# Performance work log

Hardware: AMD Instinct MI355X
Metric: run time of the kernel (lower is better)

The kernel has to match this reference:

```python
import jax, jax.numpy as jnp
import numpy as np


def _banded_diag_mean(a, b, r):
    """For each (batch i, row j) return mean of (a[i] @ b[i].T)[j, j-r:j+r+1],
    computed without materializing the LxL matrix. Windows are clipped to
    [max(0,j-r), min(L, j+r+1)].  a, b: [B, L, D]."""
    B, L, _ = a.shape
    sums = jnp.zeros((B, L), a.dtype)
    counts = jnp.zeros((L,), a.dtype)
    for d in range(-r, r + 1):  # small fixed set of 2r+1 diagonals
        if d >= 0:
            dots = jnp.einsum('bld,bld->bl', a[:, :L - d], b[:, d:])
            sums = sums.at[:, :L - d].add(dots)
            counts = counts.at[:L - d].add(1.0)
        else:
            dots = jnp.einsum('bld,bld->bl', a[:, -d:], b[:, :L + d])
            sums = sums.at[:, -d:].add(dots)
            counts = counts.at[-d:].add(1.0)
    return sums / counts


def setup_inputs() -> dict:
    key = jax.random.key(0)
    k1, k2, k3 = jax.random.split(key, 3)
    B, L, D_in, D_feat = 8, 1024, 512, 256
    return {
        'feature1': jax.random.normal(k1, (B, L, D_in), jnp.float32),
        'feature2': jax.random.normal(k2, (B, L, D_in), jnp.float32),
        'W': jax.random.normal(k3, (D_in, D_feat), jnp.float32) / np.sqrt(D_in),
        'b': jnp.zeros((D_feat,), jnp.float32),
        'positive_range_self': 4,
        'positive_range_tgt': 4,
    }


def reference(feature1, feature2, W, b, positive_range_self, positive_range_tgt):
    # MLPLayer projection (shared eval_func for both inputs): linear + relu
    emb_1 = jax.nn.relu(feature1 @ W + b)  # [B, L, Df]
    emb_2 = jax.nn.relu(feature2 @ W + b)  # [B, L, Df]
    B, L, Df = emb_1.shape
    N = B * L

    positive = jnp.einsum('bld,bld->bl', emb_1, emb_2)  # [B, L]
    if positive_range_self > 0:
        positive = positive + _banded_diag_mean(emb_1, emb_1, positive_range_self)
        positive = positive + _banded_diag_mean(emb_2, emb_2, positive_range_self)
    if positive_range_tgt > 0:
        positive = positive + _banded_diag_mean(emb_1, emb_2, positive_range_tgt)
    positive = positive.reshape(N)

    e1 = emb_1.reshape(N, Df)
    e2 = emb_2.reshape(N, Df)
    sim_matrix = e1 @ e2.T  # [N, N]
    negative = jax.nn.logsumexp(sim_matrix, axis=-1) - jnp.log(jnp.asarray(N, sim_matrix.dtype))

    nce_loss = jnp.mean(-positive + negative)
    return nce_loss
```

## Files before the change

### kernel.cpp

```cpp
#include <hip/hip_runtime.h>
#include <hip/hip_bf16.h>
#include <math.h>

#define DIN 512
#define DF 256
#define LSEQ 1024
#define NTOT 8192

typedef __attribute__((ext_vector_type(8))) short short8;
typedef __attribute__((ext_vector_type(4))) short short4v;
typedef __attribute__((ext_vector_type(4))) float f32x4;

__device__ __forceinline__ short f2bf(float x) {
  union { float f; unsigned u; } un; un.f = x;
  unsigned r = un.u + 0x7fffu + ((un.u >> 16) & 1u);
  return (short)(r >> 16);
}
__device__ __forceinline__ float bf2f(short s) {
  union { unsigned u; float f; } un; un.u = ((unsigned)(unsigned short)s) << 16;
  return un.f;
}

typedef __attribute__((address_space(1))) const unsigned char AS1c;
typedef __attribute__((address_space(3))) unsigned char AS3;
__device__ __forceinline__ void gload16(const void* g, void* l) {
  __builtin_amdgcn_global_load_lds((AS1c*)g, (AS3*)l, 16, 0, 0);
}
#define CFENCE() asm volatile("" ::: "memory")
#define LN2 0.69314718056f

__global__ __launch_bounds__(256) void prep_w_kernel(const float* __restrict__ W,
                                                     short* __restrict__ Wt) {
  __shared__ short t[64 * 70];
  const int tid = threadIdx.x;
  const int k0 = (blockIdx.x & 7) * 64;
  const int c0 = (blockIdx.x >> 3) * 64;
  const int cl = tid & 63, kq = tid >> 6;
#pragma unroll
  for (int r = 0; r < 16; ++r) {
    int kl = kq * 16 + r;
    t[cl * 70 + kl] = f2bf(W[(size_t)(k0 + kl) * DF + c0 + cl]);
  }
  __syncthreads();
  const int kl2 = tid & 63, cq = tid >> 6;
#pragma unroll
  for (int r = 0; r < 16; ++r) {
    int cl2 = cq * 16 + r;
    Wt[(size_t)(c0 + cl2) * DIN + k0 + kl2] = t[cl2 * 70 + kl2];
  }
}

#define PBM 64
#define PBK 64

__global__ __launch_bounds__(256) void proj_kernel(const float* __restrict__ f1,
                                                   const float* __restrict__ f2,
                                                   const short* __restrict__ Wt,
                                                   const float* __restrict__ bias,
                                                   short* __restrict__ emb1,
                                                   short* __restrict__ emb2) {
  const float* feat = blockIdx.y ? f2 : f1;
  short* emb = blockIdx.y ? emb2 : emb1;
  __shared__ short ldsA[8 * 64 * 8];
  __shared__ short ldsB[8 * 256 * 8];
  const int tid = threadIdx.x;
  const int lane = tid & 63, wv = tid >> 6;
  const int wrow = (wv & 1) * 32, wcol = (wv >> 1) * 128;
  const int l15 = lane & 15, lk16 = lane >> 4;
  const int rowbase = blockIdx.x * PBM;

  f32x4 acc[2][8];
#pragma unroll
  for (int mi = 0; mi < 2; ++mi)
#pragma unroll
    for (int nf = 0; nf < 8; ++nf) acc[mi][nf] = f32x4{0.f, 0.f, 0.f, 0.f};

  for (int K0 = 0; K0 < DIN; K0 += PBK) {
    __syncthreads();
#pragma unroll
    for (int i = 0; i < 8; ++i)
      gload16(Wt + (size_t)tid * DIN + K0 + i * 8, ldsB + (i * 256 + tid) * 8);
#pragma unroll
    for (int i = 0; i < 2; ++i) {
      int g = i * 256 + tid;
      int kb = g >> 6, r = g & 63;
      const float* src = feat + (size_t)(rowbase + r) * DIN + K0 + kb * 8;
      f32x4 v0 = *(const f32x4*)(src);
      f32x4 v1 = *(const f32x4*)(src + 4);
      short8 h;
      h[0] = f2bf(v0[0]); h[1] = f2bf(v0[1]); h[2] = f2bf(v0[2]); h[3] = f2bf(v0[3]);
      h[4] = f2bf(v1[0]); h[5] = f2bf(v1[1]); h[6] = f2bf(v1[2]); h[7] = f2bf(v1[3]);
      *(short8*)(ldsA + g * 8) = h;
    }
    __syncthreads();
#pragma unroll
    for (int kk = 0; kk < 2; ++kk) {
      const int kb = kk * 4 + lk16;
      short8 af[2], bf[8];
#pragma unroll
      for (int mi = 0; mi < 2; ++mi)
        af[mi] = *(const short8*)(ldsA + (kb * 64 + wrow + mi * 16 + l15) * 8);
#pragma unroll
      for (int nf = 0; nf < 8; ++nf)
        bf[nf] = *(const short8*)(ldsB + (kb * 256 + wcol + nf * 16 + l15) * 8);
#pragma unroll
      for (int mi = 0; mi < 2; ++mi)
#pragma unroll
        for (int nf = 0; nf < 8; ++nf)
          acc[mi][nf] = __builtin_amdgcn_mfma_f32_16x16x32_bf16(af[mi], bf[nf], acc[mi][nf], 0, 0, 0);
    }
  }
  const int r4 = (lane >> 4) * 4;
#pragma unroll
  for (int mi = 0; mi < 2; ++mi) {
    int row0 = rowbase + wrow + mi * 16 + r4;
#pragma unroll
    for (int nf = 0; nf < 8; ++nf) {
      int col = wcol + nf * 16 + l15;
      float bb = bias[col];
#pragma unroll
      for (int r = 0; r < 4; ++r) {
        float v = acc[mi][nf][r] + bb;
        v = v > 0.f ? v : 0.f;
        emb[(size_t)(row0 + r) * DF + col] = f2bf(v);
      }
    }
  }
}

#define POSR 32
#define PSTR 258

__global__ __launch_bounds__(256) void positive_kernel(const short* __restrict__ emb1,
                                                       const short* __restrict__ emb2,
                                                       const int* __restrict__ prs,
                                                       const int* __restrict__ prt,
                                                       float* __restrict__ pos) {
  __shared__ short s1[40 * PSTR];
  __shared__ short s2[40 * PSTR];
  const int tid = threadIdx.x;
  const int b = blockIdx.x >> 5;
  const int j0 = (blockIdx.x & 31) * POSR;
  const int rs = prs[0], rt = prt[0];

  {
    const int rr = tid >> 6, c4 = (tid & 63) * 4;
#pragma unroll
    for (int it = 0; it < 10; ++it) {
      int r = it * 4 + rr;
      int g = j0 - 4 + r;
      short4v v1 = short4v{0, 0, 0, 0}, v2 = short4v{0, 0, 0, 0};
      if (g >= 0 && g < LSEQ) {
        size_t off = (size_t)(b * LSEQ + g) * DF + c4;
        v1 = *(const short4v*)(emb1 + off);
        v2 = *(const short4v*)(emb2 + off);
      }
      *(short4v*)(s1 + r * PSTR + c4) = v1;
      *(short4v*)(s2 + r * PSTR + c4) = v2;
    }
  }
  __syncthreads();

  const int lane = tid & 63, wv = tid >> 6;
  for (int q = 0; q < 8; ++q) {
    const int j = j0 + wv * 8 + q;
    const int rl = wv * 8 + q + 4;
    float a1[4], a2[4];
    {
      short4v v1 = *(const short4v*)(s1 + rl * PSTR + lane * 4);
      short4v v2 = *(const short4v*)(s2 + rl * PSTR + lane * 4);
#pragma unroll
      for (int i = 0; i < 4; ++i) { a1[i] = bf2f(v1[i]); a2[i] = bf2f(v2[i]); }
    }
    float dot12 = 0.f, p11 = 0.f, p22 = 0.f, p12 = 0.f;
#pragma unroll
    for (int i = 0; i < 4; ++i) dot12 += a1[i] * a2[i];
    int rmax = rs > rt ? rs : rt;
    for (int d = -rmax; d <= rmax; ++d) {
      int k = j + d;
      if (k < 0 || k >= LSEQ) continue;
      int kl = rl + d;
      short4v w1 = *(const short4v*)(s1 + kl * PSTR + lane * 4);
      short4v w2 = *(const short4v*)(s2 + kl * PSTR + lane * 4);
      float d11 = 0.f, d22 = 0.f, d12 = 0.f;
#pragma unroll
      for (int i = 0; i < 4; ++i) {
        float e1k = bf2f(w1[i]), e2k = bf2f(w2[i]);
        d11 += a1[i] * e1k;
        d22 += a2[i] * e2k;
        d12 += a1[i] * e2k;
      }
      if (d >= -rs && d <= rs) { p11 += d11; p22 += d22; }
      if (d >= -rt && d <= rt) { p12 += d12; }
    }
#pragma unroll
    for (int m = 1; m < 64; m <<= 1) {
      dot12 += __shfl_xor(dot12, m);
      p11 += __shfl_xor(p11, m);
      p22 += __shfl_xor(p22, m);
      p12 += __shfl_xor(p12, m);
    }
    if (lane == 0) {
      float res = dot12;
      if (rs > 0) {
        int lo = j - rs < 0 ? 0 : j - rs;
        int hi = j + rs > LSEQ - 1 ? LSEQ - 1 : j + rs;
        res += (p11 + p22) / (float)(hi - lo + 1);
      }
      if (rt > 0) {
        int lo = j - rt < 0 ? 0 : j - rt;
        int hi = j + rt > LSEQ - 1 ? LSEQ - 1 : j + rt;
        res += p12 / (float)(hi - lo + 1);
      }
      pos[b * LSEQ + j] = res;
    }
  }
}

#define NBM 128
#define NBN 32
#define NCHUNK 16
#define CHW (NTOT / NCHUNK)
#define NT (CHW / NBN)

__global__ __launch_bounds__(256, 3) void negative_kernel(const short* __restrict__ e1,
                                                          const short* __restrict__ e2,
                                                          float* __restrict__ mpart,
                                                          float* __restrict__ spart) {
  __shared__ short ldsB[2][NBN * DF];
  const int tid = threadIdx.x;
  const int lane = tid & 63, wv = tid >> 6;
  const int l15 = lane & 15, lk16 = lane >> 4;
  const int rowbase = blockIdx.x * NBM + wv * 32;
  const short* colbase = e2 + (size_t)(blockIdx.y * CHW) * DF;

  const int src_off = (tid & 31) * DF + (tid >> 5) * 8;
  const int dst_off = wv * 512;

  auto stage = [&](int tt) {
    const short* nb = colbase + (size_t)tt * NBN * DF + src_off;
    short* db = (short*)ldsB[tt & 1] + dst_off;
#pragma unroll
    for (int i = 0; i < 4; ++i)
      gload16(nb + i * 64, db + i * 2048);
  };

  stage(0);
  CFENCE();
  short8 a[2][8];
#pragma unroll
  for (int mi = 0; mi < 2; ++mi)
#pragma unroll
    for (int ks = 0; ks < 8; ++ks)
      a[mi][ks] = *(const short8*)(e1 + (size_t)(rowbase + mi * 16 + l15) * DF + ks * 32 + lk16 * 8);
  CFENCE();
  stage(1);
  CFENCE();

  float mrun[8], srun[8];
#pragma unroll
  for (int i = 0; i < 8; ++i) { mrun[i] = -1e30f; srun[i] = 0.f; }

  for (int t = 0; t < NT; ++t) {
    if (t < NT - 1) asm volatile("s_waitcnt vmcnt(4)" ::: "memory");
    else            asm volatile("s_waitcnt vmcnt(0)" ::: "memory");
    __builtin_amdgcn_s_barrier();
    const short* bbase = (const short*)ldsB[t & 1] + lk16 * 256 + l15 * 8;

    f32x4 acc[2][2];
#pragma unroll
    for (int mi = 0; mi < 2; ++mi)
#pragma unroll
      for (int nf = 0; nf < 2; ++nf) acc[mi][nf] = f32x4{0.f, 0.f, 0.f, 0.f};

    __builtin_amdgcn_s_setprio(1);
#pragma unroll
    for (int ks = 0; ks < 8; ++ks) {
      short8 b0 = *(const short8*)(bbase + ks * 1024);
      short8 b1 = *(const short8*)(bbase + ks * 1024 + 128);
#pragma unroll
      for (int mi = 0; mi < 2; ++mi) {
        acc[mi][0] = __builtin_amdgcn_mfma_f32_16x16x32_bf16(a[mi][ks], b0, acc[mi][0], 0, 0, 0);
        acc[mi][1] = __builtin_amdgcn_mfma_f32_16x16x32_bf16(a[mi][ks], b1, acc[mi][1], 0, 0, 0);
      }
    }
    __builtin_amdgcn_s_setprio(0);

#pragma unroll
    for (int mi = 0; mi < 2; ++mi)
#pragma unroll
      for (int r = 0; r < 4; ++r) {
        int s8 = mi * 4 + r;
        float v0 = acc[mi][0][r], v1 = acc[mi][1][r];
        float mo = mrun[s8];
        float mn = fmaxf(mo, fmaxf(v0, v1));
        mrun[s8] = mn;
        srun[s8] = srun[s8] * __expf(mo - mn) + __expf(v0 - mn) + __expf(v1 - mn);
      }
    __builtin_amdgcn_s_barrier();
    CFENCE();
    if (t + 2 < NT) stage(t + 2);
  }

#pragma unroll
  for (int mi = 0; mi < 2; ++mi)
#pragma unroll
    for (int r = 0; r < 4; ++r) {
      int s8 = mi * 4 + r;
      float m = mrun[s8], s = srun[s8];
#pragma unroll
      for (int msk = 1; msk < 16; msk <<= 1) {
        float mo = __shfl_xor(m, msk);
        float so = __shfl_xor(s, msk);
        float mn = fmaxf(m, mo);
        s = s * __expf(m - mn) + so * __expf(mo - mn);
        m = mn;
      }
      if (l15 == 0) {
        int row = rowbase + mi * 16 + lk16 * 4 + r;
        mpart[blockIdx.y * NTOT + row] = m;
        spart[blockIdx.y * NTOT + row] = s;
      }
    }
}

__global__ __launch_bounds__(256) void finalize1_kernel(const float* __restrict__ pos,
                                                        const float* __restrict__ mpart,
                                                        const float* __restrict__ spart,
                                                        float* __restrict__ partial) {
  __shared__ float red[4];
  int row = blockIdx.x * 256 + threadIdx.x;
  float m = -1e30f;
#pragma unroll
  for (int c = 0; c < NCHUNK; ++c) m = fmaxf(m, mpart[c * NTOT + row]);
  float s = 0.f;
#pragma unroll
  for (int c = 0; c < NCHUNK; ++c) s += spart[c * NTOT + row] * __expf(mpart[c * NTOT + row] - m);
  float v = m + LN2 * __builtin_amdgcn_logf(s) - pos[row];
#pragma unroll
  for (int msk = 1; msk < 64; msk <<= 1) v += __shfl_xor(v, msk);
  if ((threadIdx.x & 63) == 0) red[threadIdx.x >> 6] = v;
  __syncthreads();
  if (threadIdx.x == 0) partial[blockIdx.x] = red[0] + red[1] + red[2] + red[3];
}

__global__ __launch_bounds__(64) void finalize2_kernel(const float* __restrict__ partial,
                                                       float* __restrict__ out) {
  int lane = threadIdx.x;
  float v = lane < 32 ? partial[lane] : 0.f;
#pragma unroll
  for (int msk = 1; msk < 64; msk <<= 1) v += __shfl_xor(v, msk);
  if (lane == 0) out[0] = v / (float)NTOT - logf((float)NTOT);
}

extern "C" void kernel_launch(void* const* d_in, const int* in_sizes, int n_in,
                              void* d_out, int out_size, void* d_ws, size_t ws_size,
                              hipStream_t stream) {
  const float* f1 = (const float*)d_in[0];
  const float* f2 = (const float*)d_in[1];
  const float* W = (const float*)d_in[2];
  const float* bias = (const float*)d_in[3];
  const int* prs = (const int*)d_in[4];
  const int* prt = (const int*)d_in[5];
  float* out = (float*)d_out;

  char* ws = (char*)d_ws;
  short* Wt = (short*)(ws);
  short* emb1 = (short*)(ws + 262144);
  short* emb2 = (short*)(ws + 262144 + 4194304);
  float* pos = (float*)(ws + 8650752);
  float* mpart = (float*)(ws + 8683520);
  float* spart = (float*)(ws + 9207808);
  float* partial = (float*)(ws + 9732096);

  prep_w_kernel<<<32, 256, 0, stream>>>(W, Wt);
  proj_kernel<<<dim3(NTOT / PBM, 2), 256, 0, stream>>>(f1, f2, Wt, bias, emb1, emb2);
  positive_kernel<<<NTOT / POSR, 256, 0, stream>>>(emb1, emb2, prs, prt, pos);
  negative_kernel<<<dim3(NTOT / NBM, NCHUNK), 256, 0, stream>>>(emb1, emb2, mpart, spart);
  finalize1_kernel<<<32, 256, 0, stream>>>(pos, mpart, spart, partial);
  finalize2_kernel<<<1, 64, 0, stream>>>(partial, out);
}
```

Before: 96.70 us.

## Replace async LDS double buffer with register-staged prefetch and swizzled 64-column tiles

```diff
diff --git a/kernel.cpp b/kernel.cpp
--- a/kernel.cpp
+++ b/kernel.cpp
@@ -218,90 +218,98 @@
 }
 
 #define NBM 128
-#define NBN 32
+#define NBN 64
 #define NCHUNK 16
 #define CHW (NTOT / NCHUNK)
 #define NT (CHW / NBN)
 
-__global__ __launch_bounds__(256, 3) void negative_kernel(const short* __restrict__ e1,
-                                                          const short* __restrict__ e2,
-                                                          float* __restrict__ mpart,
-                                                          float* __restrict__ spart) {
-  __shared__ short ldsB[2][NBN * DF];
+__global__ __launch_bounds__(256) void negative_kernel(const short* __restrict__ e1,
+                                                       const short* __restrict__ e2,
+                                                       float* __restrict__ mpart,
+                                                       float* __restrict__ spart) {
+  __shared__ short ldsB[NBN * DF];
   const int tid = threadIdx.x;
   const int lane = tid & 63, wv = tid >> 6;
   const int l15 = lane & 15, lk16 = lane >> 4;
-  const int rowbase = blockIdx.x * NBM + wv * 32;
-  const short* colbase = e2 + (size_t)(blockIdx.y * CHW) * DF;
-
-  const int src_off = (tid & 31) * DF + (tid >> 5) * 8;
-  const int dst_off = wv * 512;
-
-  auto stage = [&](int tt) {
-    const short* nb = colbase + (size_t)tt * NBN * DF + src_off;
-    short* db = (short*)ldsB[tt & 1] + dst_off;
-#pragma unroll
-    for (int i = 0; i < 4; ++i)
-      gload16(nb + i * 64, db + i * 2048);
-  };
-
-  stage(0);
-  CFENCE();
+  const int rb = blockIdx.x, chunk = blockIdx.y;
+  const int rowbase = rb * NBM + wv * 32;
+  const int colbase0 = chunk * CHW;
+
   short8 a[2][8];
 #pragma unroll
   for (int mi = 0; mi < 2; ++mi)
 #pragma unroll
     for (int ks = 0; ks < 8; ++ks)
       a[mi][ks] = *(const short8*)(e1 + (size_t)(rowbase + mi * 16 + l15) * DF + ks * 32 + lk16 * 8);
-  CFENCE();
-  stage(1);
-  CFENCE();
 
   float mrun[8], srun[8];
 #pragma unroll
   for (int i = 0; i < 8; ++i) { mrun[i] = -1e30f; srun[i] = 0.f; }
 
+  short8 st[8];
+  {
+    const short* src = e2 + (size_t)colbase0 * DF;
+#pragma unroll
+    for (int it = 0; it < 8; ++it) {
+      int S = it * 256 + tid;
+      int c = S >> 5, kblk = S & 31;
+      st[it] = *(const short8*)(src + (size_t)c * DF + kblk * 8);
+    }
+  }
   for (int t = 0; t < NT; ++t) {
-    if (t < NT - 1) asm volatile("s_waitcnt vmcnt(4)" ::: "memory");
-    else            asm volatile("s_waitcnt vmcnt(0)" ::: "memory");
-    __builtin_amdgcn_s_barrier();
-    const short* bbase = (const short*)ldsB[t & 1] + lk16 * 256 + l15 * 8;
-
-    f32x4 acc[2][2];
+    __syncthreads();
+#pragma unroll
+    for (int it = 0; it < 8; ++it) {
+      int S = it * 256 + tid;
+      int c = S >> 5, kblk = S & 31;
+      int slot = kblk ^ (c & 7);
+      *(short8*)(ldsB + (c * 32 + slot) * 8) = st[it];
+    }
+    __syncthreads();
+    if (t + 1 < NT) {
+      const short* src = e2 + (size_t)(colbase0 + (t + 1) * NBN) * DF;
+#pragma unroll
+      for (int it = 0; it < 8; ++it) {
+        int S = it * 256 + tid;
+        int c = S >> 5, kblk = S & 31;
+        st[it] = *(const short8*)(src + (size_t)c * DF + kblk * 8);
+      }
+    }
+    f32x4 acc[2][4];
 #pragma unroll
     for (int mi = 0; mi < 2; ++mi)
 #pragma unroll
-      for (int nf = 0; nf < 2; ++nf) acc[mi][nf] = f32x4{0.f, 0.f, 0.f, 0.f};
-
-    __builtin_amdgcn_s_setprio(1);
+      for (int nf = 0; nf < 4; ++nf) acc[mi][nf] = f32x4{0.f, 0.f, 0.f, 0.f};
 #pragma unroll
     for (int ks = 0; ks < 8; ++ks) {
-      short8 b0 = *(const short8*)(bbase + ks * 1024);
-      short8 b1 = *(const short8*)(bbase + ks * 1024 + 128);
-#pragma unroll
-      for (int mi = 0; mi < 2; ++mi) {
-        acc[mi][0] = __builtin_amdgcn_mfma_f32_16x16x32_bf16(a[mi][ks], b0, acc[mi][0], 0, 0, 0);
-        acc[mi][1] = __builtin_amdgcn_mfma_f32_16x16x32_bf16(a[mi][ks], b1, acc[mi][1], 0, 0, 0);
-      }
-    }
-    __builtin_amdgcn_s_setprio(0);
-
+      short8 bfr[4];
+#pragma unroll
+      for (int nf = 0; nf < 4; ++nf) {
+        int c = nf * 16 + l15;
+        int kblk = ks * 4 + lk16;
+        int slot = kblk ^ (c & 7);
+        bfr[nf] = *(const short8*)(ldsB + (c * 32 + slot) * 8);
+      }
+#pragma unroll
+      for (int mi = 0; mi < 2; ++mi)
+#pragma unroll
+        for (int nf = 0; nf < 4; ++nf)
+          acc[mi][nf] = __builtin_amdgcn_mfma_f32_16x16x32_bf16(a[mi][ks], bfr[nf], acc[mi][nf], 0, 0, 0);
+    }
 #pragma unroll
     for (int mi = 0; mi < 2; ++mi)
 #pragma unroll
       for (int r = 0; r < 4; ++r) {
         int s8 = mi * 4 + r;
-        float v0 = acc[mi][0][r], v1 = acc[mi][1][r];
-        float mo = mrun[s8];
-        float mn = fmaxf(mo, fmaxf(v0, v1));
+        float v0 = acc[mi][0][r], v1 = acc[mi][1][r], v2 = acc[mi][2][r], v3 = acc[mi][3][r];
+        float mx = fmaxf(fmaxf(v0, v1), fmaxf(v2, v3));
+        float mn = fmaxf(mrun[s8], mx);
+        float sc = __expf(mrun[s8] - mn);
+        float sm = __expf(v0 - mn) + __expf(v1 - mn) + __expf(v2 - mn) + __expf(v3 - mn);
+        srun[s8] = srun[s8] * sc + sm;
         mrun[s8] = mn;
-        srun[s8] = srun[s8] * __expf(mo - mn) + __expf(v0 - mn) + __expf(v1 - mn);
-      }
-    __builtin_amdgcn_s_barrier();
-    CFENCE();
-    if (t + 2 < NT) stage(t + 2);
-  }
-
+      }
+  }
 #pragma unroll
   for (int mi = 0; mi < 2; ++mi)
 #pragma unroll
@@ -318,8 +326,8 @@
       }
       if (l15 == 0) {
         int row = rowbase + mi * 16 + lk16 * 4 + r;
-        mpart[blockIdx.y * NTOT + row] = m;
-        spart[blockIdx.y * NTOT + row] = s;
+        mpart[chunk * NTOT + row] = m;
+        spart[chunk * NTOT + row] = s;
       }
     }
 }
```

After: 96.65 us. About the same (-0.1%).
